# Kernel optimization log

Hardware: AMD Instinct MI355X
Metric: run time of the kernel (lower is better)

The kernel has to match this reference:

```python
import jax, jax.numpy as jnp
import numpy as np

N_NODES = 10000
N_EDGES = 320000
D_IN = 256
D_HID = 256
N_CLASSES = 40


def _init_linear(key, fan_in, fan_out):
    kw, kb = jax.random.split(key)
    bound = 1.0 / np.sqrt(fan_in)
    W = jax.random.uniform(kw, (fan_in, fan_out), jnp.float32, -bound, bound)
    b = jax.random.uniform(kb, (fan_out,), jnp.float32, -bound, bound)
    return W, b


def setup_inputs() -> dict:
    key = jax.random.key(0)
    k0, k1, k2, k3, k4 = jax.random.split(key, 5)
    node_features = jax.random.normal(k0, (N_NODES, D_IN), jnp.float32)
    edge_index = jax.random.randint(k1, (2, N_EDGES), 0, N_NODES, jnp.int64)
    W1, b1 = _init_linear(k2, D_IN, D_HID)
    W2, b2 = _init_linear(k3, D_HID, D_HID)
    W3, b3 = _init_linear(k4, D_HID, N_CLASSES)
    return {"node_features": node_features, "edge_index": edge_index,
            "W1": W1, "b1": b1, "W2": W2, "b2": b2, "W3": W3, "b3": b3}


def _mp_layer(x, src, dst, W, b):
    # message: linear transform of source-node features (transform-then-gather
    # is mathematically identical to gather-then-transform and cheaper when E>N)
    msg = (x @ W + b)[src]                      # [E, d_out]
    # scatter sum-aggregate messages at destination nodes
    out = jax.ops.segment_sum(msg, dst, num_segments=N_NODES)  # [N, d_out]
    return out


def reference(node_features, edge_index, W1, b1, W2, b2, W3, b3):
    src, dst = edge_index[0], edge_index[1]
    x = jax.nn.relu(_mp_layer(node_features, src, dst, W1, b1))
    x = jax.nn.relu(_mp_layer(x, src, dst, W2, b2))
    x = jax.nn.relu(_mp_layer(x, src, dst, W3, b3))
    return x
```

## Files before the change

### kernel.cpp

```cpp
#include <hip/hip_runtime.h>


#define N_NODES   10000
#define N_EDGES   320000
#define D_HID     256
#define N_CLASSES 40
#define NSB       10
#define CAP_S     24
#define DUMMY     10000

typedef __attribute__((ext_vector_type(8))) short short8;
typedef __attribute__((ext_vector_type(4))) float f32x4;

__device__ __forceinline__ ushort f2bf(float f) {
    unsigned u = __float_as_uint(f);
    u = (u + 0x7fffu + ((u >> 16) & 1u)) >> 16;
    return (ushort)u;
}
__device__ __forceinline__ float bf2f(ushort u) {
    return __uint_as_float(((unsigned)u) << 16);
}


__global__ __launch_bounds__(256)
void prep_kernel(const float* __restrict__ X,
                 const float* __restrict__ W1, const float* __restrict__ W2,
                 const float* __restrict__ W3,
                 ushort* __restrict__ Xb, ushort* __restrict__ bufY,
                 ushort* __restrict__ bufH,
                 ushort* __restrict__ W1b, ushort* __restrict__ W2b,
                 ushort* __restrict__ W3b, int* __restrict__ cur2,
                 int* __restrict__ esrc2) {
    const int tid  = blockIdx.x * 256 + threadIdx.x;
    const int nthr = gridDim.x * 256;
    for (int i = tid; i < N_NODES * NSB; i += nthr) cur2[i] = 0;
    for (int i = tid; i < N_NODES * NSB * CAP_S; i += nthr) esrc2[i] = DUMMY;
    ushort4 z; z.x = 0; z.y = 0; z.z = 0; z.w = 0;
    if (tid < 64) {
        ((ushort4*)Xb)[640000 + tid]   = z;
        ((ushort4*)bufY)[640000 + tid] = z;
    }
    if (tid < 10) ((ushort4*)bufH)[100000 + tid] = z;
    for (int i = tid; i < N_NODES * D_HID / 4; i += nthr) {
        float4 v = ((const float4*)X)[i];
        ushort4 o;
        o.x = f2bf(v.x); o.y = f2bf(v.y); o.z = f2bf(v.z); o.w = f2bf(v.w);
        ((ushort4*)Xb)[i] = o;
    }
    for (int i = tid; i < 141312; i += nthr) {
        if (i < 65536) {
            int n = i >> 8, k = i & 255;
            W1b[i] = f2bf(W1[k * 256 + n]);
        } else if (i < 131072) {
            int t2 = i - 65536;
            int n = t2 >> 8, k = t2 & 255;
            W2b[t2] = f2bf(W2[k * 256 + n]);
        } else {
            int t2 = i - 131072;
            int n = t2 >> 8, k = t2 & 255;
            W3b[t2] = f2bf(W3[k * N_CLASSES + n]);
        }
    }
}


__global__ __launch_bounds__(256)
void place_kernel(const int* __restrict__ edges, int* __restrict__ cur2,
                  int* __restrict__ esrc2) {
    int e = blockIdx.x * 256 + threadIdx.x;
    if (e < N_EDGES) {
        int s = edges[e];
        int d = edges[N_EDGES + e];
        int sb = s >> 10;
        int bin = d * NSB + sb;
        int pos = atomicAdd(&cur2[bin], 1);
        if (pos < CAP_S) esrc2[bin * CAP_S + pos] = s;
    }
}


__global__ __launch_bounds__(256)
void gather_kernel(const ushort* __restrict__ Xin, const int* __restrict__ cur2,
                   const int* __restrict__ esrc2, ushort* __restrict__ Ag,
                   float* __restrict__ degOut) {
    __shared__ int eidx[4 * NSB * CAP_S];
    __shared__ int cnts[4 * NSB];

    const int tid  = threadIdx.x;
    const int w    = tid >> 6, lane = tid & 63;
    const int lo   = lane & 31, hi = lane >> 5;
    const int base = blockIdx.x * 4;

    for (int i = tid; i < 4 * NSB * CAP_S; i += 256)
        eidx[i] = esrc2[base * NSB * CAP_S + i];
    if (tid < 4 * NSB) cnts[tid] = cur2[base * NSB + tid];
    __syncthreads();

    const int node = base + w;
    const uint4* hp4 = (const uint4*)Xin;
    float a[8] = {};
    int degT = 0;
    for (int sb = 0; sb < NSB; ++sb) {
        int raw = cnts[w * NSB + sb];
        degT += raw;
        int cnt = raw < CAP_S ? raw : CAP_S;
        const int* ep = eidx + (w * NSB + sb) * CAP_S;
        for (int b = 0; b < cnt; b += 4) {
            int e0 = ep[b + hi];
            int e1 = ep[b + 2 + hi];
            uint4 v0 = hp4[(size_t)e0 * 32 + lo];
            uint4 v1 = hp4[(size_t)e1 * 32 + lo];
            a[0] += bf2f((ushort)(v0.x & 0xffff)); a[1] += bf2f((ushort)(v0.x >> 16));
            a[2] += bf2f((ushort)(v0.y & 0xffff)); a[3] += bf2f((ushort)(v0.y >> 16));
            a[4] += bf2f((ushort)(v0.z & 0xffff)); a[5] += bf2f((ushort)(v0.z >> 16));
            a[6] += bf2f((ushort)(v0.w & 0xffff)); a[7] += bf2f((ushort)(v0.w >> 16));
            a[0] += bf2f((ushort)(v1.x & 0xffff)); a[1] += bf2f((ushort)(v1.x >> 16));
            a[2] += bf2f((ushort)(v1.y & 0xffff)); a[3] += bf2f((ushort)(v1.y >> 16));
            a[4] += bf2f((ushort)(v1.z & 0xffff)); a[5] += bf2f((ushort)(v1.z >> 16));
            a[6] += bf2f((ushort)(v1.w & 0xffff)); a[7] += bf2f((ushort)(v1.w >> 16));
        }
    }
#pragma unroll
    for (int j = 0; j < 8; ++j) a[j] += __shfl_xor(a[j], 32);
    if (lane < 32) {
        uint4 o;
        o.x = (unsigned)f2bf(a[0]) | ((unsigned)f2bf(a[1]) << 16);
        o.y = (unsigned)f2bf(a[2]) | ((unsigned)f2bf(a[3]) << 16);
        o.z = (unsigned)f2bf(a[4]) | ((unsigned)f2bf(a[5]) << 16);
        o.w = (unsigned)f2bf(a[6]) | ((unsigned)f2bf(a[7]) << 16);
        ((uint4*)(Ag + (size_t)node * 256))[lo] = o;
    }
    if (lane == 0) degOut[node] = (float)degT;
}


#define LDSB 264

template<bool CHAIN>
__global__ __launch_bounds__(512)
void gemm_kernel(const ushort* __restrict__ Ag, const ushort* __restrict__ Bt,
                 const float* __restrict__ bias, const float* __restrict__ degF,
                 const ushort* __restrict__ W3b, const float* __restrict__ b3,
                 ushort* __restrict__ Out) {
    __shared__ ushort Bs[256 * LDSB];
    __shared__ ushort W3L[40 * LDSB];
    __shared__ float  degL[64];

    const int tid  = threadIdx.x;
    const int wave = tid >> 6, lane = tid & 63;
    const int lr = lane & 15, lg = lane >> 4;
    const int rg = wave >> 1, cg = wave & 1;
    const int rowBase = blockIdx.x * 64;

#pragma unroll
    for (int p = 0; p < 16; ++p) {
        int idx = p * 512 + tid;
        int n = idx >> 5, c = (idx & 31) * 8;
        *(uint4*)(Bs + n * LDSB + c) = *(const uint4*)(Bt + (size_t)n * 256 + c);
    }
    if (CHAIN) {
#pragma unroll
        for (int p = 0; p < 3; ++p) {
            int idx = p * 512 + tid;
            if (idx < 1280) {
                int n = idx >> 5, c = (idx & 31) * 8;
                *(uint4*)(W3L + n * LDSB + c) = *(const uint4*)(W3b + (size_t)n * 256 + c);
            }
        }
    }
    if (tid < 64) degL[tid] = degF[rowBase + tid];

    short8 afr[8];
    const size_t aBase = (size_t)(rowBase + rg * 16 + lr) * 256 + lg * 8;
#pragma unroll
    for (int ks = 0; ks < 8; ++ks)
        afr[ks] = *(const short8*)(Ag + aBase + ks * 32);

    __syncthreads();

    f32x4 acc[8] = {};
#pragma unroll
    for (int ks = 0; ks < 8; ++ks) {
        int k0 = ks * 32;
#pragma unroll
        for (int j = 0; j < 8; ++j) {
            short8 bf = *(const short8*)(Bs + (cg * 128 + j * 16 + lr) * LDSB + k0 + lg * 8);
            acc[j] = __builtin_amdgcn_mfma_f32_16x16x32_bf16(afr[ks], bf, acc[j], 0, 0, 0);
        }
    }

    if (!CHAIN) {
#pragma unroll
        for (int j = 0; j < 8; ++j) {
            int col = cg * 128 + j * 16 + lr;
            float bv = bias[col];
#pragma unroll
            for (int r = 0; r < 4; ++r) {
                int rl = rg * 16 + lg * 4 + r;
                int grow = rowBase + rl;
                if (grow < N_NODES)
                    Out[(size_t)grow * 256 + col] =
                        f2bf(fmaxf(fmaf(degL[rl], bv, acc[j][r]), 0.f));
            }
        }
    } else {
        __syncthreads();
#pragma unroll
        for (int j = 0; j < 8; ++j) {
            int col = cg * 128 + j * 16 + lr;
            float bv = bias[col];
#pragma unroll
            for (int r = 0; r < 4; ++r) {
                int rl = rg * 16 + lg * 4 + r;
                Bs[rl * LDSB + col] = f2bf(fmaxf(fmaf(degL[rl], bv, acc[j][r]), 0.f));
            }
        }
        __syncthreads();
        for (int t = wave; t < 12; t += 8) {
            int rT = t & 3, cT = t >> 2;
            f32x4 a3 = {};
#pragma unroll
            for (int ks = 0; ks < 8; ++ks) {
                short8 af = *(const short8*)(Bs + (rT * 16 + lr) * LDSB + ks * 32 + lg * 8);
                short8 bf = *(const short8*)(W3L + (cT * 16 + lr) * LDSB + ks * 32 + lg * 8);
                a3 = __builtin_amdgcn_mfma_f32_16x16x32_bf16(af, bf, a3, 0, 0, 0);
            }
            int col = cT * 16 + lr;
            if (col < N_CLASSES) {
                float bv = b3[col];
#pragma unroll
                for (int r = 0; r < 4; ++r) {
                    int grow = rowBase + rT * 16 + lg * 4 + r;
                    if (grow < N_NODES)
                        Out[(size_t)grow * N_CLASSES + col] = f2bf(a3[r] + bv);
                }
            }
        }
    }
}


__global__ __launch_bounds__(256)
void agg_relu_40_kernel(const ushort* __restrict__ h, const int* __restrict__ cur2,
                        const int* __restrict__ esrc2, float* __restrict__ out) {
    const int wv   = threadIdx.x >> 6;
    const int lane = threadIdx.x & 63;
    const int node = (blockIdx.x << 2) + wv;
    const int l6   = (lane < 60) ? lane : 0;
    const int g6   = l6 / 10;
    const int c10  = l6 - g6 * 10;

    const int* cp  = cur2 + node * NSB;
    const int* ep2 = esrc2 + node * NSB * CAP_S;
    float a0 = 0.f, a1 = 0.f, a2 = 0.f, a3 = 0.f;
    for (int sb = 0; sb < NSB; ++sb) {
        int cnt = cp[sb];
        if (cnt > CAP_S) cnt = CAP_S;
        const int* ep = ep2 + sb * CAP_S;
        for (int b = 0; b < cnt; b += 6) {
            int s = ep[b + g6];
            uint2 v = *(const uint2*)(h + (size_t)s * N_CLASSES + c10 * 4);
            a0 += bf2f((ushort)(v.x & 0xffff)); a1 += bf2f((ushort)(v.x >> 16));
            a2 += bf2f((ushort)(v.y & 0xffff)); a3 += bf2f((ushort)(v.y >> 16));
        }
    }
#define FOLD40(x) { x += __shfl(x, lane + 30);                      \
                    float t1 = __shfl(x, lane + 10);                \
                    float t2 = __shfl(x, lane + 20);                \
                    x += t1 + t2; }
    FOLD40(a0); FOLD40(a1); FOLD40(a2); FOLD40(a3);
#undef FOLD40
    if (lane < 10) {
        float4 o;
        o.x = fmaxf(a0, 0.f); o.y = fmaxf(a1, 0.f);
        o.z = fmaxf(a2, 0.f); o.w = fmaxf(a3, 0.f);
        *(float4*)(out + (size_t)node * N_CLASSES + lane * 4) = o;
    }
}


extern "C" void kernel_launch(void* const* d_in, const int* in_sizes, int n_in,
                              void* d_out, int out_size, void* d_ws, size_t ws_size,
                              hipStream_t stream) {
    const float* X     = (const float*)d_in[0];
    const int*   edges = (const int*)d_in[1];
    const float* W1 = (const float*)d_in[2];
    const float* b1 = (const float*)d_in[3];
    const float* W2 = (const float*)d_in[4];
    const float* b2 = (const float*)d_in[5];
    const float* W3 = (const float*)d_in[6];
    const float* b3 = (const float*)d_in[7];
    float* out = (float*)d_out;

    char* ws = (char*)d_ws;
    ushort* Xb    = (ushort*)(ws);
    ushort* bufY  = (ushort*)(ws + 5120512);
    ushort* bufH  = (ushort*)(ws + 10241024);
    ushort* W1b   = (ushort*)(ws + 11041104);
    ushort* W2b   = (ushort*)(ws + 11172176);
    ushort* W3b   = (ushort*)(ws + 11303248);
    int*    cur2  = (int*)(ws + 11323728);
    int*    esrc2 = (int*)(ws + 11723728);
    ushort* Ag1   = (ushort*)(ws + 21323728);
    ushort* Ag2   = (ushort*)(ws + 26468304);
    float*  degF  = (float*)(ws + 31612880);

    prep_kernel<<<512, 256, 0, stream>>>(X, W1, W2, W3, Xb, bufY, bufH,
                                         W1b, W2b, W3b, cur2, esrc2);
    place_kernel<<<(N_EDGES + 255) / 256, 256, 0, stream>>>(edges, cur2, esrc2);
    gather_kernel<<<N_NODES / 4, 256, 0, stream>>>(Xb, cur2, esrc2, Ag1, degF);
    gemm_kernel<false><<<157, 512, 0, stream>>>(Ag1, W1b, b1, degF, W3b, b3, bufY);
    gather_kernel<<<N_NODES / 4, 256, 0, stream>>>(bufY, cur2, esrc2, Ag2, degF);
    gemm_kernel<true><<<157, 512, 0, stream>>>(Ag2, W2b, b2, degF, W3b, b3, bufH);
    agg_relu_40_kernel<<<N_NODES / 4, 256, 0, stream>>>(bufH, cur2, esrc2, out);
}
```

Baseline: 169.9 us.

## Replace source-binned edge buckets with flat per-destination lists and batched gathers

Drops the 10 source-bin buckets per destination node in favour of one flat adjacency list per node with capacity 96. The prep kernel no longer fills a 10M-int DUMMY array, and the gather kernel now issues 8 independent row loads per iteration, padding unused slots with the zero dummy row. It also adds a prefetch that touches the input feature rows to warm the cache. The trade-off is losing the source-locality ordering from binning, and edges beyond 96 per node are silently dropped.

```diff
diff --git a/kernel.cpp b/kernel.cpp
--- a/kernel.cpp
+++ b/kernel.cpp
@@ -5,8 +5,7 @@
 #define N_EDGES   320000
 #define D_HID     256
 #define N_CLASSES 40
-#define NSB       10
-#define CAP_S     24
+#define CAP       96
 #define DUMMY     10000
 
 typedef __attribute__((ext_vector_type(8))) short short8;
@@ -29,12 +28,10 @@
                  ushort* __restrict__ Xb, ushort* __restrict__ bufY,
                  ushort* __restrict__ bufH,
                  ushort* __restrict__ W1b, ushort* __restrict__ W2b,
-                 ushort* __restrict__ W3b, int* __restrict__ cur2,
-                 int* __restrict__ esrc2) {
+                 ushort* __restrict__ W3b, int* __restrict__ cursor) {
     const int tid  = blockIdx.x * 256 + threadIdx.x;
     const int nthr = gridDim.x * 256;
-    for (int i = tid; i < N_NODES * NSB; i += nthr) cur2[i] = 0;
-    for (int i = tid; i < N_NODES * NSB * CAP_S; i += nthr) esrc2[i] = DUMMY;
+    for (int i = tid; i < N_NODES; i += nthr) cursor[i] = 0;
     ushort4 z; z.x = 0; z.y = 0; z.z = 0; z.w = 0;
     if (tid < 64) {
         ((ushort4*)Xb)[640000 + tid]   = z;
@@ -65,59 +62,63 @@
 
 
 __global__ __launch_bounds__(256)
-void place_kernel(const int* __restrict__ edges, int* __restrict__ cur2,
-                  int* __restrict__ esrc2) {
+void place_kernel(const int* __restrict__ edges, int* __restrict__ cursor,
+                  int* __restrict__ esrc) {
     int e = blockIdx.x * 256 + threadIdx.x;
     if (e < N_EDGES) {
-        int s = edges[e];
         int d = edges[N_EDGES + e];
-        int sb = s >> 10;
-        int bin = d * NSB + sb;
-        int pos = atomicAdd(&cur2[bin], 1);
-        if (pos < CAP_S) esrc2[bin * CAP_S + pos] = s;
+        int pos = atomicAdd(&cursor[d], 1);
+        if (pos < CAP) esrc[d * CAP + pos] = edges[e];
     }
 }
 
 
 __global__ __launch_bounds__(256)
-void gather_kernel(const ushort* __restrict__ Xin, const int* __restrict__ cur2,
-                   const int* __restrict__ esrc2, ushort* __restrict__ Ag,
+void gather_kernel(const ushort* __restrict__ Xin, const int* __restrict__ deg,
+                   const int* __restrict__ esrc, ushort* __restrict__ Ag,
                    float* __restrict__ degOut) {
-    __shared__ int eidx[4 * NSB * CAP_S];
-    __shared__ int cnts[4 * NSB];
+    __shared__ int eidx[4 * CAP];
+    __shared__ int degL[4];
 
     const int tid  = threadIdx.x;
     const int w    = tid >> 6, lane = tid & 63;
     const int lo   = lane & 31, hi = lane >> 5;
     const int base = blockIdx.x * 4;
-
-    for (int i = tid; i < 4 * NSB * CAP_S; i += 256)
-        eidx[i] = esrc2[base * NSB * CAP_S + i];
-    if (tid < 4 * NSB) cnts[tid] = cur2[base * NSB + tid];
+    const uint4* hp4 = (const uint4*)Xin;
+
+    {
+        int i = blockIdx.x * 256 + tid;
+        if (i < 320000) {
+            uint4 t = hp4[i];
+            asm volatile("" :: "v"(t.x), "v"(t.y), "v"(t.z), "v"(t.w));
+        }
+    }
+
+    for (int i = tid; i < 4 * CAP; i += 256)
+        eidx[i] = esrc[base * CAP + i];
+    if (tid < 4) degL[tid] = deg[base + tid];
     __syncthreads();
 
     const int node = base + w;
-    const uint4* hp4 = (const uint4*)Xin;
+    const int raw  = degL[w];
+    const int cnt  = raw < CAP ? raw : CAP;
+    const int nb   = (cnt + 15) >> 4;
+
     float a[8] = {};
-    int degT = 0;
-    for (int sb = 0; sb < NSB; ++sb) {
-        int raw = cnts[w * NSB + sb];
-        degT += raw;
-        int cnt = raw < CAP_S ? raw : CAP_S;
-        const int* ep = eidx + (w * NSB + sb) * CAP_S;
-        for (int b = 0; b < cnt; b += 4) {
-            int e0 = ep[b + hi];
-            int e1 = ep[b + 2 + hi];
-            uint4 v0 = hp4[(size_t)e0 * 32 + lo];
-            uint4 v1 = hp4[(size_t)e1 * 32 + lo];
-            a[0] += bf2f((ushort)(v0.x & 0xffff)); a[1] += bf2f((ushort)(v0.x >> 16));
-            a[2] += bf2f((ushort)(v0.y & 0xffff)); a[3] += bf2f((ushort)(v0.y >> 16));
-            a[4] += bf2f((ushort)(v0.z & 0xffff)); a[5] += bf2f((ushort)(v0.z >> 16));
-            a[6] += bf2f((ushort)(v0.w & 0xffff)); a[7] += bf2f((ushort)(v0.w >> 16));
-            a[0] += bf2f((ushort)(v1.x & 0xffff)); a[1] += bf2f((ushort)(v1.x >> 16));
-            a[2] += bf2f((ushort)(v1.y & 0xffff)); a[3] += bf2f((ushort)(v1.y >> 16));
-            a[4] += bf2f((ushort)(v1.z & 0xffff)); a[5] += bf2f((ushort)(v1.z >> 16));
-            a[6] += bf2f((ushort)(v1.w & 0xffff)); a[7] += bf2f((ushort)(v1.w >> 16));
+    for (int b = 0; b < nb; ++b) {
+        uint4 v[8];
+#pragma unroll
+        for (int u = 0; u < 8; ++u) {
+            int slot = b * 16 + 2 * u + hi;
+            int e = (slot < cnt) ? eidx[w * CAP + slot] : DUMMY;
+            v[u] = hp4[(size_t)e * 32 + lo];
+        }
+#pragma unroll
+        for (int u = 0; u < 8; ++u) {
+            a[0] += bf2f((ushort)(v[u].x & 0xffff)); a[1] += bf2f((ushort)(v[u].x >> 16));
+            a[2] += bf2f((ushort)(v[u].y & 0xffff)); a[3] += bf2f((ushort)(v[u].y >> 16));
+            a[4] += bf2f((ushort)(v[u].z & 0xffff)); a[5] += bf2f((ushort)(v[u].z >> 16));
+            a[6] += bf2f((ushort)(v[u].w & 0xffff)); a[7] += bf2f((ushort)(v[u].w >> 16));
         }
     }
 #pragma unroll
@@ -130,7 +131,7 @@
         o.w = (unsigned)f2bf(a[6]) | ((unsigned)f2bf(a[7]) << 16);
         ((uint4*)(Ag + (size_t)node * 256))[lo] = o;
     }
-    if (lane == 0) degOut[node] = (float)degT;
+    if (lane == 0) degOut[node] = (float)raw;
 }
 
 
@@ -241,8 +242,8 @@
 
 
 __global__ __launch_bounds__(256)
-void agg_relu_40_kernel(const ushort* __restrict__ h, const int* __restrict__ cur2,
-                        const int* __restrict__ esrc2, float* __restrict__ out) {
+void agg_relu_40_kernel(const ushort* __restrict__ h, const int* __restrict__ deg,
+                        const int* __restrict__ esrc, float* __restrict__ out) {
     const int wv   = threadIdx.x >> 6;
     const int lane = threadIdx.x & 63;
     const int node = (blockIdx.x << 2) + wv;
@@ -250,19 +251,16 @@
     const int g6   = l6 / 10;
     const int c10  = l6 - g6 * 10;
 
-    const int* cp  = cur2 + node * NSB;
-    const int* ep2 = esrc2 + node * NSB * CAP_S;
+    int cnt = deg[node];
+    if (cnt > CAP) cnt = CAP;
+    const int* ep = esrc + node * CAP;
     float a0 = 0.f, a1 = 0.f, a2 = 0.f, a3 = 0.f;
-    for (int sb = 0; sb < NSB; ++sb) {
-        int cnt = cp[sb];
-        if (cnt > CAP_S) cnt = CAP_S;
-        const int* ep = ep2 + sb * CAP_S;
-        for (int b = 0; b < cnt; b += 6) {
-            int s = ep[b + g6];
-            uint2 v = *(const uint2*)(h + (size_t)s * N_CLASSES + c10 * 4);
-            a0 += bf2f((ushort)(v.x & 0xffff)); a1 += bf2f((ushort)(v.x >> 16));
-            a2 += bf2f((ushort)(v.y & 0xffff)); a3 += bf2f((ushort)(v.y >> 16));
-        }
+    for (int b = 0; b < cnt; b += 6) {
+        int slot = b + g6;
+        int s = (slot < cnt) ? ep[slot] : DUMMY;
+        uint2 v = *(const uint2*)(h + (size_t)s * N_CLASSES + c10 * 4);
+        a0 += bf2f((ushort)(v.x & 0xffff)); a1 += bf2f((ushort)(v.x >> 16));
+        a2 += bf2f((ushort)(v.y & 0xffff)); a3 += bf2f((ushort)(v.y >> 16));
     }
 #define FOLD40(x) { x += __shfl(x, lane + 30);                      \
                     float t1 = __shfl(x, lane + 10);                \
@@ -299,18 +297,18 @@
     ushort* W1b   = (ushort*)(ws + 11041104);
     ushort* W2b   = (ushort*)(ws + 11172176);
     ushort* W3b   = (ushort*)(ws + 11303248);
-    int*    cur2  = (int*)(ws + 11323728);
-    int*    esrc2 = (int*)(ws + 11723728);
-    ushort* Ag1   = (ushort*)(ws + 21323728);
-    ushort* Ag2   = (ushort*)(ws + 26468304);
-    float*  degF  = (float*)(ws + 31612880);
+    int*    cursor= (int*)(ws + 11323728);
+    int*    esrc  = (int*)(ws + 11363728);
+    ushort* Ag1   = (ushort*)(ws + 15203728);
+    ushort* Ag2   = (ushort*)(ws + 20348304);
+    float*  degF  = (float*)(ws + 25492880);
 
     prep_kernel<<<512, 256, 0, stream>>>(X, W1, W2, W3, Xb, bufY, bufH,
-                                         W1b, W2b, W3b, cur2, esrc2);
-    place_kernel<<<(N_EDGES + 255) / 256, 256, 0, stream>>>(edges, cur2, esrc2);
-    gather_kernel<<<N_NODES / 4, 256, 0, stream>>>(Xb, cur2, esrc2, Ag1, degF);
+                                         W1b, W2b, W3b, cursor);
+    place_kernel<<<(N_EDGES + 255) / 256, 256, 0, stream>>>(edges, cursor, esrc);
+    gather_kernel<<<N_NODES / 4, 256, 0, stream>>>(Xb, cursor, esrc, Ag1, degF);
     gemm_kernel<false><<<157, 512, 0, stream>>>(Ag1, W1b, b1, degF, W3b, b3, bufY);
-    gather_kernel<<<N_NODES / 4, 256, 0, stream>>>(bufY, cur2, esrc2, Ag2, degF);
+    gather_kernel<<<N_NODES / 4, 256, 0, stream>>>(bufY, cursor, esrc, Ag2, degF);
     gemm_kernel<true><<<157, 512, 0, stream>>>(Ag2, W2b, b2, degF, W3b, b3, bufH);
-    agg_relu_40_kernel<<<N_NODES / 4, 256, 0, stream>>>(bufH, cur2, esrc2, out);
-}
+    agg_relu_40_kernel<<<N_NODES / 4, 256, 0, stream>>>(bufH, cursor, esrc, out);
+}
```

Measured after the change: 159.2 us. -6.3%, faster.

## Shrink edge bins to two source halves with padded counters and wider gathers

Applied to the files above, without the earlier changes.

Edges are now binned per destination into two source-half bins of capacity 48 instead of ten bins of capacity 24. Bin counters are padded to a 16-int stride so atomics on different bins do not share cache lines. The source list is no longer pre-filled with dummies; unused slots are masked at read time. The gather loop issues eight row loads per iteration to raise memory-level parallelism. In exchange, the memset work and bin-padding loads shrink, but locality by source block is coarser and a bin holding more than 48 edges would silently drop them.

```diff
diff --git a/kernel.cpp b/kernel.cpp
--- a/kernel.cpp
+++ b/kernel.cpp
@@ -5,8 +5,9 @@
 #define N_EDGES   320000
 #define D_HID     256
 #define N_CLASSES 40
-#define NSB       10
-#define CAP_S     24
+#define NSB       2
+#define CAP2      48
+#define CSTRIDE   16
 #define DUMMY     10000
 
 typedef __attribute__((ext_vector_type(8))) short short8;
@@ -29,12 +30,10 @@
                  ushort* __restrict__ Xb, ushort* __restrict__ bufY,
                  ushort* __restrict__ bufH,
                  ushort* __restrict__ W1b, ushort* __restrict__ W2b,
-                 ushort* __restrict__ W3b, int* __restrict__ cur2,
-                 int* __restrict__ esrc2) {
+                 ushort* __restrict__ W3b, int* __restrict__ cur2) {
     const int tid  = blockIdx.x * 256 + threadIdx.x;
     const int nthr = gridDim.x * 256;
-    for (int i = tid; i < N_NODES * NSB; i += nthr) cur2[i] = 0;
-    for (int i = tid; i < N_NODES * NSB * CAP_S; i += nthr) esrc2[i] = DUMMY;
+    for (int i = tid; i < N_NODES * NSB * CSTRIDE; i += nthr) cur2[i] = 0;
     ushort4 z; z.x = 0; z.y = 0; z.z = 0; z.w = 0;
     if (tid < 64) {
         ((ushort4*)Xb)[640000 + tid]   = z;
@@ -71,10 +70,9 @@
     if (e < N_EDGES) {
         int s = edges[e];
         int d = edges[N_EDGES + e];
-        int sb = s >> 10;
-        int bin = d * NSB + sb;
-        int pos = atomicAdd(&cur2[bin], 1);
-        if (pos < CAP_S) esrc2[bin * CAP_S + pos] = s;
+        int bin = d * NSB + (s >= 5000 ? 1 : 0);
+        int pos = atomicAdd(&cur2[bin * CSTRIDE], 1);
+        if (pos < CAP2) esrc2[bin * CAP2 + pos] = s;
     }
 }
 
@@ -83,7 +81,7 @@
 void gather_kernel(const ushort* __restrict__ Xin, const int* __restrict__ cur2,
                    const int* __restrict__ esrc2, ushort* __restrict__ Ag,
                    float* __restrict__ degOut) {
-    __shared__ int eidx[4 * NSB * CAP_S];
+    __shared__ int eidx[4 * NSB * CAP2];
     __shared__ int cnts[4 * NSB];
 
     const int tid  = threadIdx.x;
@@ -91,33 +89,36 @@
     const int lo   = lane & 31, hi = lane >> 5;
     const int base = blockIdx.x * 4;
 
-    for (int i = tid; i < 4 * NSB * CAP_S; i += 256)
-        eidx[i] = esrc2[base * NSB * CAP_S + i];
-    if (tid < 4 * NSB) cnts[tid] = cur2[base * NSB + tid];
+    for (int i = tid; i < 4 * NSB * CAP2; i += 256)
+        eidx[i] = esrc2[base * NSB * CAP2 + i];
+    if (tid < 4 * NSB) cnts[tid] = cur2[(base * NSB + tid) * CSTRIDE];
     __syncthreads();
 
     const int node = base + w;
     const uint4* hp4 = (const uint4*)Xin;
     float a[8] = {};
     int degT = 0;
+#pragma unroll
     for (int sb = 0; sb < NSB; ++sb) {
         int raw = cnts[w * NSB + sb];
         degT += raw;
-        int cnt = raw < CAP_S ? raw : CAP_S;
-        const int* ep = eidx + (w * NSB + sb) * CAP_S;
-        for (int b = 0; b < cnt; b += 4) {
-            int e0 = ep[b + hi];
-            int e1 = ep[b + 2 + hi];
-            uint4 v0 = hp4[(size_t)e0 * 32 + lo];
-            uint4 v1 = hp4[(size_t)e1 * 32 + lo];
-            a[0] += bf2f((ushort)(v0.x & 0xffff)); a[1] += bf2f((ushort)(v0.x >> 16));
-            a[2] += bf2f((ushort)(v0.y & 0xffff)); a[3] += bf2f((ushort)(v0.y >> 16));
-            a[4] += bf2f((ushort)(v0.z & 0xffff)); a[5] += bf2f((ushort)(v0.z >> 16));
-            a[6] += bf2f((ushort)(v0.w & 0xffff)); a[7] += bf2f((ushort)(v0.w >> 16));
-            a[0] += bf2f((ushort)(v1.x & 0xffff)); a[1] += bf2f((ushort)(v1.x >> 16));
-            a[2] += bf2f((ushort)(v1.y & 0xffff)); a[3] += bf2f((ushort)(v1.y >> 16));
-            a[4] += bf2f((ushort)(v1.z & 0xffff)); a[5] += bf2f((ushort)(v1.z >> 16));
-            a[6] += bf2f((ushort)(v1.w & 0xffff)); a[7] += bf2f((ushort)(v1.w >> 16));
+        int cnt = raw < CAP2 ? raw : CAP2;
+        const int* ep = eidx + (w * NSB + sb) * CAP2;
+        for (int b = 0; b < cnt; b += 16) {
+            uint4 v[8];
+#pragma unroll
+            for (int u = 0; u < 8; ++u) {
+                int slot = b + 2 * u + hi;
+                int e = (slot < cnt) ? ep[slot] : DUMMY;
+                v[u] = hp4[(size_t)e * 32 + lo];
+            }
+#pragma unroll
+            for (int u = 0; u < 8; ++u) {
+                a[0] += bf2f((ushort)(v[u].x & 0xffff)); a[1] += bf2f((ushort)(v[u].x >> 16));
+                a[2] += bf2f((ushort)(v[u].y & 0xffff)); a[3] += bf2f((ushort)(v[u].y >> 16));
+                a[4] += bf2f((ushort)(v[u].z & 0xffff)); a[5] += bf2f((ushort)(v[u].z >> 16));
+                a[6] += bf2f((ushort)(v[u].w & 0xffff)); a[7] += bf2f((ushort)(v[u].w >> 16));
+            }
         }
     }
 #pragma unroll
@@ -250,15 +251,15 @@
     const int g6   = l6 / 10;
     const int c10  = l6 - g6 * 10;
 
-    const int* cp  = cur2 + node * NSB;
-    const int* ep2 = esrc2 + node * NSB * CAP_S;
     float a0 = 0.f, a1 = 0.f, a2 = 0.f, a3 = 0.f;
+#pragma unroll
     for (int sb = 0; sb < NSB; ++sb) {
-        int cnt = cp[sb];
-        if (cnt > CAP_S) cnt = CAP_S;
-        const int* ep = ep2 + sb * CAP_S;
+        int cnt = cur2[(node * NSB + sb) * CSTRIDE];
+        if (cnt > CAP2) cnt = CAP2;
+        const int* ep = esrc2 + (node * NSB + sb) * CAP2;
         for (int b = 0; b < cnt; b += 6) {
-            int s = ep[b + g6];
+            int slot = b + g6;
+            int s = (slot < cnt) ? ep[slot] : DUMMY;
             uint2 v = *(const uint2*)(h + (size_t)s * N_CLASSES + c10 * 4);
             a0 += bf2f((ushort)(v.x & 0xffff)); a1 += bf2f((ushort)(v.x >> 16));
             a2 += bf2f((ushort)(v.y & 0xffff)); a3 += bf2f((ushort)(v.y >> 16));
@@ -300,13 +301,13 @@
     ushort* W2b   = (ushort*)(ws + 11172176);
     ushort* W3b   = (ushort*)(ws + 11303248);
     int*    cur2  = (int*)(ws + 11323728);
-    int*    esrc2 = (int*)(ws + 11723728);
-    ushort* Ag1   = (ushort*)(ws + 21323728);
-    ushort* Ag2   = (ushort*)(ws + 26468304);
-    float*  degF  = (float*)(ws + 31612880);
+    int*    esrc2 = (int*)(ws + 12603728);
+    ushort* Ag1   = (ushort*)(ws + 16443728);
+    ushort* Ag2   = (ushort*)(ws + 21588304);
+    float*  degF  = (float*)(ws + 26732880);
 
     prep_kernel<<<512, 256, 0, stream>>>(X, W1, W2, W3, Xb, bufY, bufH,
-                                         W1b, W2b, W3b, cur2, esrc2);
+                                         W1b, W2b, W3b, cur2);
     place_kernel<<<(N_EDGES + 255) / 256, 256, 0, stream>>>(edges, cur2, esrc2);
     gather_kernel<<<N_NODES / 4, 256, 0, stream>>>(Xb, cur2, esrc2, Ag1, degF);
     gemm_kernel<false><<<157, 512, 0, stream>>>(Ag1, W1b, b1, degF, W3b, b3, bufY);
```

Result: faster. 152.4 us (-10.3%).
